# Performance work log

Measured on AMD Instinct MI355X. Metric: run time of the kernel, lower is better.

## Reference

```python
import jax, jax.numpy as jnp
import numpy as np

NUM_CELLS = 16384
NUM_CLASSES = 64
BATCH = 64


def setup_inputs() -> dict:
    key = jax.random.key(0)
    k1, k2 = jax.random.split(key)
    x = jax.random.normal(k1, (BATCH, NUM_CELLS, 1), dtype=jnp.float32)
    weights = jax.random.normal(k2, (NUM_CELLS, NUM_CLASSES, 3), dtype=jnp.float32)
    bias = jnp.zeros((NUM_CELLS, NUM_CLASSES), dtype=jnp.float32)
    return {"x": x, "weights": weights, "bias": bias}


def reference(x, weights, bias):
    # x: (B, N, 1); weights: (N, C, 3); bias: (N, C)
    xs = x[..., 0]                      # (B, N)
    left = jnp.roll(xs, 1, axis=1)      # x[:, i-1]
    right = jnp.roll(xs, -1, axis=1)    # x[:, i+1]
    # out[b,i,c] = left*W[i,c,0] + center*W[i,c,1] + right*W[i,c,2] + bias[i,c]
    out = (left[:, :, None] * weights[:, :, 0]
           + xs[:, :, None] * weights[:, :, 1]
           + right[:, :, None] * weights[:, :, 2]
           + bias)
    return 1.7159 * jnp.tanh(out * (2.0 / 3.0))
```

## Files before the change

### kernel.cpp

```cpp
#include <hip/hip_runtime.h>

#define N_CELLS   16384
#define N_CLASSES 64
#define BATCH     64
#define CPB       128

typedef float f32x4 __attribute__((ext_vector_type(4)));
typedef float f32x2 __attribute__((ext_vector_type(2)));

#define K_EXP 1.9235933878f

__device__ __forceinline__ float agm_act(float s) {
    float e = __builtin_amdgcn_exp2f(-K_EXP * fabsf(s));
    float r = __builtin_amdgcn_rcpf(1.0f + e);
    return copysignf(fmaf(3.4318f, r, -1.7159f), s);
}

__global__ __launch_bounds__(256) void mnl_kernel(
    const float* __restrict__ x,
    const float* __restrict__ w,
    const float* __restrict__ bias,
    float* __restrict__ out)
{
    const int bid   = blockIdx.x;
    const int b     = bid >> 7;
    const int chunk = bid & 127;
    const int i0    = chunk * CPB;
    const int t     = threadIdx.x;

    const float* __restrict__ xb = x + (size_t)b * N_CELLS;
    float* __restrict__ ob = out + (size_t)b * N_CELLS * N_CLASSES
                                 + (size_t)i0 * N_CLASSES;

    #pragma unroll 4
    for (int it = 0; it < 8; ++it) {
        const int slot = it * 256 + t;
        const int cell = slot >> 4;
        const int quad = slot & 15;
        const int i    = i0 + cell;

        const int il = (i == 0)           ? N_CELLS - 1 : i - 1;
        const int ir = (i == N_CELLS - 1) ? 0           : i + 1;

        const float xl = xb[il];
        const float xc = xb[i];
        const float xr = xb[ir];

        const float4* wv = reinterpret_cast<const float4*>(
            w + (size_t)i * (N_CLASSES * 3) + (size_t)quad * 12);
        const float4 v0 = wv[0], v1 = wv[1], v2 = wv[2];
        const float4 bi = *reinterpret_cast<const float4*>(
            bias + (size_t)i * N_CLASSES + quad * 4);

        f32x4 o;
        o.x = agm_act(fmaf(xl, v0.x, fmaf(xc, v0.y, fmaf(xr, v0.z, bi.x))));
        o.y = agm_act(fmaf(xl, v0.w, fmaf(xc, v1.x, fmaf(xr, v1.y, bi.y))));
        o.z = agm_act(fmaf(xl, v1.z, fmaf(xc, v1.w, fmaf(xr, v2.x, bi.z))));
        o.w = agm_act(fmaf(xl, v2.y, fmaf(xc, v2.z, fmaf(xr, v2.w, bi.w))));

        f32x4* op = reinterpret_cast<f32x4*>(ob + (size_t)slot * 4);
        __builtin_nontemporal_store(o, op);
    }
}

extern "C" void kernel_launch(void* const* d_in, const int* in_sizes, int n_in,
                              void* d_out, int out_size, void* d_ws, size_t ws_size,
                              hipStream_t stream) {
    const float* x    = (const float*)d_in[0];
    const float* w    = (const float*)d_in[1];
    const float* bias = (const float*)d_in[2];
    float* out = (float*)d_out;

    dim3 grid(BATCH * (N_CELLS / CPB));
    dim3 block(256);
    mnl_kernel<<<grid, block, 0, stream>>>(x, w, bias, out);
}
```

Measured before the change: 63.63 us.

## Hold weights in registers and loop over batches to reuse them

Each thread now loads its weight and bias vectors once and iterates over 16 batch indices, instead of reloading weights for every batch. Blocks cover 16 cells and a quarter of the batches, with a fixed grid of 4096. This cuts repeated weight reads from cache/HBM, while stores remain the dominant traffic and are now spread across strided batch locations.

Measured after the change: 66.85 us. +5.1%, slower.

```diff
diff --git a/kernel.cpp b/kernel.cpp
--- a/kernel.cpp
+++ b/kernel.cpp
@@ -3,10 +3,8 @@
 #define N_CELLS   16384
 #define N_CLASSES 64
 #define BATCH     64
-#define CPB       128
 
 typedef float f32x4 __attribute__((ext_vector_type(4)));
-typedef float f32x2 __attribute__((ext_vector_type(2)));
 
 #define K_EXP 1.9235933878f
 
@@ -22,35 +20,31 @@
     const float* __restrict__ bias,
     float* __restrict__ out)
 {
-    const int bid   = blockIdx.x;
-    const int b     = bid >> 7;
-    const int chunk = bid & 127;
-    const int i0    = chunk * CPB;
-    const int t     = threadIdx.x;
+    const int bid  = blockIdx.x;
+    const int t    = threadIdx.x;
+    const int i0   = (bid & 1023) * 16;
+    const int bq   = bid >> 10;
+    const int cell = t >> 4;
+    const int quad = t & 15;
+    const int i    = i0 + cell;
 
-    const float* __restrict__ xb = x + (size_t)b * N_CELLS;
-    float* __restrict__ ob = out + (size_t)b * N_CELLS * N_CLASSES
-                                 + (size_t)i0 * N_CLASSES;
+    const int il = (i == 0)           ? N_CELLS - 1 : i - 1;
+    const int ir = (i == N_CELLS - 1) ? 0           : i + 1;
+
+    const float4* wv = reinterpret_cast<const float4*>(
+        w + (size_t)i * (N_CLASSES * 3) + (size_t)quad * 12);
+    const float4 v0 = wv[0], v1 = wv[1], v2 = wv[2];
+    const float4 bi = *reinterpret_cast<const float4*>(
+        bias + (size_t)i * N_CLASSES + quad * 4);
 
     #pragma unroll 4
-    for (int it = 0; it < 8; ++it) {
-        const int slot = it * 256 + t;
-        const int cell = slot >> 4;
-        const int quad = slot & 15;
-        const int i    = i0 + cell;
+    for (int p = 0; p < 16; ++p) {
+        const int b = p * 4 + bq;
+        const size_t xb = (size_t)b * N_CELLS;
 
-        const int il = (i == 0)           ? N_CELLS - 1 : i - 1;
-        const int ir = (i == N_CELLS - 1) ? 0           : i + 1;
-
-        const float xl = xb[il];
-        const float xc = xb[i];
-        const float xr = xb[ir];
-
-        const float4* wv = reinterpret_cast<const float4*>(
-            w + (size_t)i * (N_CLASSES * 3) + (size_t)quad * 12);
-        const float4 v0 = wv[0], v1 = wv[1], v2 = wv[2];
-        const float4 bi = *reinterpret_cast<const float4*>(
-            bias + (size_t)i * N_CLASSES + quad * 4);
+        const float xl = x[xb + il];
+        const float xc = x[xb + i];
+        const float xr = x[xb + ir];
 
         f32x4 o;
         o.x = agm_act(fmaf(xl, v0.x, fmaf(xc, v0.y, fmaf(xr, v0.z, bi.x))));
@@ -58,7 +52,8 @@
         o.z = agm_act(fmaf(xl, v1.z, fmaf(xc, v1.w, fmaf(xr, v2.x, bi.z))));
         o.w = agm_act(fmaf(xl, v2.y, fmaf(xc, v2.z, fmaf(xr, v2.w, bi.w))));
 
-        f32x4* op = reinterpret_cast<f32x4*>(ob + (size_t)slot * 4);
+        f32x4* op = reinterpret_cast<f32x4*>(
+            out + ((size_t)b * N_CELLS + i) * N_CLASSES + quad * 4);
         __builtin_nontemporal_store(o, op);
     }
 }
@@ -71,7 +66,7 @@
     const float* bias = (const float*)d_in[2];
     float* out = (float*)d_out;
 
-    dim3 grid(BATCH * (N_CELLS / CPB));
+    dim3 grid(4096);
     dim3 block(256);
     mnl_kernel<<<grid, block, 0, stream>>>(x, w, bias, out);
 }
```
